# Kernel optimization log

Measured on AMD Instinct MI355X. Metric: run time of the kernel, lower is better.

## Reference

```python
import jax, jax.numpy as jnp
import numpy as np

NEG_SLOPE = 0.2
LN_EPS = 1e-5


def setup_inputs() -> dict:
    key = jax.random.key(0)
    ks = jax.random.split(key, 8)
    N, F, d, L, H = 100000, 128, 64, 3, 4
    dh = d // H
    E = 1600000
    return {
        "x": jax.random.normal(ks[0], (N, F), dtype=jnp.float32),
        "edge_index": jax.random.randint(ks[1], (2, E), 0, N, dtype=jnp.int64),
        "W_enc": jax.random.normal(ks[2], (F, d), dtype=jnp.float32) / np.sqrt(F),
        "b_enc": jnp.zeros((d,), jnp.float32),
        "Wl": jax.random.normal(ks[3], (L, d, d), dtype=jnp.float32) / np.sqrt(d),
        "bl": jnp.zeros((L, d), jnp.float32),
        "Wr": jax.random.normal(ks[4], (L, d, d), dtype=jnp.float32) / np.sqrt(d),
        "br": jnp.zeros((L, d), jnp.float32),
        "att": jax.random.normal(ks[5], (L, H, dh), dtype=jnp.float32) / np.sqrt(dh),
        "out_bias": jnp.zeros((L, d), jnp.float32),
        "gamma": jnp.ones((L, d), jnp.float32),
        "beta": jnp.zeros((L, d), jnp.float32),
    }


def _elu(x):
    return jnp.where(x > 0, x, jnp.expm1(x))


def reference(x, edge_index, W_enc, b_enc, Wl, bl, Wr, br, att, out_bias, gamma, beta):
    N = x.shape[0]
    L, H, dh = att.shape
    d = H * dh
    # PyG GATv2Conv default add_self_loops=True
    loops = jnp.arange(N, dtype=edge_index.dtype)
    src = jnp.concatenate([edge_index[0], loops])  # message source
    dst = jnp.concatenate([edge_index[1], loops])  # aggregation target

    h = jax.nn.relu(x @ W_enc + b_enc)  # [N, d]
    for l in range(L):
        xl = (h @ Wl[l] + bl[l]).reshape(N, H, dh)
        xr = (h @ Wr[l] + br[l]).reshape(N, H, dh)
        # GATv2: score = a^T LeakyReLU(xl[src] + xr[dst])  -> [E, H]
        e = jax.nn.leaky_relu(xl[src] + xr[dst], NEG_SLOPE)
        score = jnp.einsum('ehd,hd->eh', e, att[l])
        # segment softmax over incoming edges of each dst node
        smax = jax.ops.segment_max(score, dst, num_segments=N)
        ex = jnp.exp(score - smax[dst])
        denom = jax.ops.segment_sum(ex, dst, num_segments=N)
        alpha = ex / denom[dst]  # [E, H]
        agg = jax.ops.segment_sum(alpha[:, :, None] * xl[src], dst, num_segments=N)
        hc = agg.reshape(N, d) + out_bias[l]
        # LayerNorm
        mu = hc.mean(-1, keepdims=True)
        var = ((hc - mu) ** 2).mean(-1, keepdims=True)
        hn = (hc - mu) * jax.lax.rsqrt(var + LN_EPS) * gamma[l] + beta[l]
        h = _elu(hn)  # dropout p=0.0 -> identity
    return h
```

## Files before the change

kernel.cpp:

```cpp
#include <hip/hip_runtime.h>
#include <hip/hip_fp16.h>
#include <math.h>

static constexpr int D = 64;
static constexpr int F = 128;
static constexpr int BK = 64;
static constexpr float NEG_SLOPE = 0.2f;
static constexpr float LN_EPS = 1e-5f;
static constexpr float LOG2E = 1.44269504088896340736f;
static constexpr int NCHUNK = 8;

template <int CTRL>
__device__ __forceinline__ float dpp_add(float x) {
  int v = __builtin_amdgcn_update_dpp(0, __float_as_int(x), CTRL, 0xF, 0xF, true);
  return x + __int_as_float(v);
}
__device__ __forceinline__ float red8(float x) {
  x = dpp_add<0xB1>(x);
  x = dpp_add<0x4E>(x);
  x = dpp_add<0x141>(x);
  return x;
}
__device__ __forceinline__ float red16(float x) {
  x = red8(x);
  x = dpp_add<0x140>(x);
  return x;
}
__device__ __forceinline__ float red32(float x) {
  x = red16(x);
  x += __shfl_xor(x, 16);
  return x;
}

__device__ __forceinline__ __half2 h2max(__half2 a, __half2 b) {
  int ai = __builtin_bit_cast(int, a), bi = __builtin_bit_cast(int, b), r;
  asm("v_pk_max_f16 %0, %1, %2" : "=v"(r) : "v"(ai), "v"(bi));
  return __builtin_bit_cast(__half2, r);
}

typedef _Float16 half2_t __attribute__((ext_vector_type(2)));
__device__ __forceinline__ float fdot2f(__half2 a, __half2 b) {
#if __has_builtin(__builtin_amdgcn_fdot2)
  return __builtin_amdgcn_fdot2(__builtin_bit_cast(half2_t, a),
                                __builtin_bit_cast(half2_t, b), 0.f, false);
#else
  float2 af = __half22float2(a), bf = __half22float2(b);
  return fmaf(af.x, bf.x, af.y * bf.y);
#endif
}


__global__ __launch_bounds__(256) void k_init_buckets(int* __restrict__ cursor,
                                                      int* __restrict__ ssrc, int N) {
  int tid = blockIdx.x * 256 + threadIdx.x;
  int total = N * (BK / 4) + 4;
  if (tid < total) {
    int row = tid >> 4;
    int sub = tid & 15;
    int4 v = make_int4(0, 0, 0, 0);
    if (sub == 0 && row < N) v.x = row;
    ((int4*)ssrc)[tid] = v;
  }
  if (tid < N) cursor[tid] = 1;
}

__global__ __launch_bounds__(256) void k_scatter(const int* __restrict__ src,
                                                 const int* __restrict__ dst,
                                                 int* __restrict__ cursor,
                                                 int* __restrict__ ssrc, int E, int N) {
  int c = blockIdx.x & (NCHUNK - 1);
  int b0 = (c * N) / NCHUNK, b1 = ((c + 1) * N) / NCHUNK;
  int stride = (gridDim.x / NCHUNK) * 256;
  for (int e = (blockIdx.x >> 3) * 256 + threadIdx.x; e < E; e += stride) {
    int d = dst[e];
    if (d >= b0 && d < b1) {
      int p = atomicAdd(&cursor[d], 1);
      if (p < BK) ssrc[(d << 6) + p] = src[e];
    }
  }
}


__global__ __launch_bounds__(256) void k_encoder(const float* __restrict__ x,
                                                 const float* __restrict__ W,
                                                 const float* __restrict__ b,
                                                 float* __restrict__ h, int N) {
  __shared__ float xT[F][64];
  __shared__ float Ws[F][64];
  int t = threadIdx.x;
  int n0 = blockIdx.x * 64;
  for (int i = t; i < F * D / 4; i += 256)
    ((float4*)&Ws[0][0])[i] = ((const float4*)W)[i];
  {
    int r = t & 63, kq = (t >> 6) * 4;
    int n = n0 + r;
#pragma unroll
    for (int i = 0; i < 8; ++i) {
      int k0 = kq + 16 * i;
      float4 v = (n < N) ? *(const float4*)&x[(size_t)n * F + k0]
                         : make_float4(0.f, 0.f, 0.f, 0.f);
      xT[k0][r] = v.x; xT[k0 + 1][r] = v.y; xT[k0 + 2][r] = v.z; xT[k0 + 3][r] = v.w;
    }
  }
  __syncthreads();
  int c4 = (t & 15) * 4, n4 = (t >> 4) * 4;
  float acc[4][4];
#pragma unroll
  for (int i = 0; i < 4; ++i)
#pragma unroll
    for (int j = 0; j < 4; ++j) acc[i][j] = b[c4 + j];
#pragma unroll 4
  for (int k = 0; k < F; ++k) {
    float4 xv = *(const float4*)&xT[k][n4];
    float4 wv = *(const float4*)&Ws[k][c4];
    const float* xp = (const float*)&xv;
    const float* wp = (const float*)&wv;
#pragma unroll
    for (int i = 0; i < 4; ++i)
#pragma unroll
      for (int j = 0; j < 4; ++j) acc[i][j] = fmaf(xp[i], wp[j], acc[i][j]);
  }
#pragma unroll
  for (int i = 0; i < 4; ++i) {
    int n = n0 + n4 + i;
    if (n < N) {
      float4 o = make_float4(fmaxf(acc[i][0], 0.f), fmaxf(acc[i][1], 0.f),
                             fmaxf(acc[i][2], 0.f), fmaxf(acc[i][3], 0.f));
      *(float4*)&h[(size_t)n * D + c4] = o;
    }
  }
}


__global__ __launch_bounds__(256) void k_layer_gemm(const float* __restrict__ h,
                                                    const float* __restrict__ Wl,
                                                    const float* __restrict__ bl,
                                                    const float* __restrict__ Wr,
                                                    const float* __restrict__ br,
                                                    ushort* __restrict__ xlh,
                                                    float* __restrict__ xr, int N) {
  __shared__ float hT[D][64];
  __shared__ float Wls[D][64];
  __shared__ float Wrs[D][64];
  int t = threadIdx.x;
  int n0 = blockIdx.x * 64;
  for (int i = t; i < D * D / 4; i += 256) {
    ((float4*)&Wls[0][0])[i] = ((const float4*)Wl)[i];
    ((float4*)&Wrs[0][0])[i] = ((const float4*)Wr)[i];
  }
  {
    int r = t & 63, kq = (t >> 6) * 4;
    int n = n0 + r;
#pragma unroll
    for (int i = 0; i < 4; ++i) {
      int k0 = kq + 16 * i;
      float4 v = (n < N) ? *(const float4*)&h[(size_t)n * D + k0]
                         : make_float4(0.f, 0.f, 0.f, 0.f);
      hT[k0][r] = v.x; hT[k0 + 1][r] = v.y; hT[k0 + 2][r] = v.z; hT[k0 + 3][r] = v.w;
    }
  }
  __syncthreads();
  int c4 = (t & 15) * 4, n4 = (t >> 4) * 4;
  float aL[4][4], aR[4][4];
#pragma unroll
  for (int i = 0; i < 4; ++i)
#pragma unroll
    for (int j = 0; j < 4; ++j) { aL[i][j] = bl[c4 + j]; aR[i][j] = br[c4 + j]; }
#pragma unroll 4
  for (int k = 0; k < D; ++k) {
    float4 xv = *(const float4*)&hT[k][n4];
    float4 lv = *(const float4*)&Wls[k][c4];
    float4 rv = *(const float4*)&Wrs[k][c4];
    const float* xp = (const float*)&xv;
    const float* lp = (const float*)&lv;
    const float* rp = (const float*)&rv;
#pragma unroll
    for (int i = 0; i < 4; ++i)
#pragma unroll
      for (int j = 0; j < 4; ++j) {
        aL[i][j] = fmaf(xp[i], lp[j], aL[i][j]);
        aR[i][j] = fmaf(xp[i], rp[j], aR[i][j]);
      }
  }
#pragma unroll
  for (int i = 0; i < 4; ++i) {
    int n = n0 + n4 + i;
    if (n < N) {
      ushort4 o;
      o.x = __half_as_ushort(__float2half_rn(aL[i][0]));
      o.y = __half_as_ushort(__float2half_rn(aL[i][1]));
      o.z = __half_as_ushort(__float2half_rn(aL[i][2]));
      o.w = __half_as_ushort(__float2half_rn(aL[i][3]));
      *(ushort4*)&xlh[(size_t)n * D + c4] = o;
      *(float4*)&xr[(size_t)n * D + c4] =
          make_float4(aR[i][0], aR[i][1], aR[i][2], aR[i][3]);
    }
  }
}


template <int P>
__device__ __forceinline__ void batchH(const char* __restrict__ xlb,
                                       const int* __restrict__ srow,
                                       int slot0, int cnt, int voff, int nd,
                                       __half2 xr2, __half2 a2, __half2 ns2,
                                       float& m, float& s, float& a0, float& a1) {
  int sj[P];
#pragma unroll
  for (int g = 0; g < P / 4; ++g) {
    int4 q = *(const int4*)(srow + slot0 + 4 * g);
    sj[4 * g + 0] = q.x; sj[4 * g + 1] = q.y;
    sj[4 * g + 2] = q.z; sj[4 * g + 3] = q.w;
  }
#pragma unroll
  for (int j = 0; j < P; ++j)
    if (slot0 + j >= cnt) sj[j] = nd;
  __half2 xsv[P];
  float p[P];
#pragma unroll
  for (int j = 0; j < P; ++j)
    xsv[j] = *(const __half2*)(xlb + (((uint32_t)sj[j] << 7) | (uint32_t)voff));
#pragma unroll
  for (int j = 0; j < P; ++j) {
    __half2 v2 = __hadd2(xsv[j], xr2);
    __half2 lr2 = h2max(v2, __hmul2(v2, ns2));
    float pj = red8(fdot2f(a2, lr2));
    p[j] = (slot0 + j < cnt) ? pj : -3.0e38f;
  }
  float pmax = p[0];
#pragma unroll
  for (int j = 1; j < P; ++j) pmax = fmaxf(pmax, p[j]);
  float mnew = fmaxf(m, pmax);
  float c = __builtin_amdgcn_exp2f(m - mnew);
  s *= c; a0 *= c; a1 *= c;
#pragma unroll
  for (int j = 0; j < P; ++j) {
    float w = __builtin_amdgcn_exp2f(p[j] - mnew);
    s += w;
    a0 = fmaf(w, __low2float(xsv[j]), a0);
    a1 = fmaf(w, __high2float(xsv[j]), a1);
  }
  m = mnew;
}

__global__ __launch_bounds__(256) void k_edge_layer(const __half* __restrict__ xlh,
                                                    const float* __restrict__ xr,
                                                    const int* __restrict__ cnt_arr,
                                                    const int* __restrict__ ssrc,
                                                    const float* __restrict__ att_l,
                                                    const float* __restrict__ ob_l,
                                                    const float* __restrict__ g_l,
                                                    const float* __restrict__ be_l,
                                                    float* __restrict__ out, int N) {
  int lane = threadIdx.x & 63;
  int c2 = lane & 31, half = lane >> 5;
  int voff = c2 * 4;
  int wid = threadIdx.x >> 6;
  int wave = blockIdx.x * 4 + wid;
  int nw = gridDim.x * 4;
  const char* xlb = (const char*)xlh;
  float2 af = make_float2(att_l[2 * c2] * LOG2E, att_l[2 * c2 + 1] * LOG2E);
  __half2 a2 = __float22half2_rn(af);
  __half2 ns2 = __float2half2_rn(NEG_SLOPE);
  float2 ob = *(const float2*)&ob_l[2 * c2];
  float2 gm = *(const float2*)&g_l[2 * c2];
  float2 bt = *(const float2*)&be_l[2 * c2];
  int npairs = (N + 1) >> 1;
  for (int ip = wave; ip < npairs; ip += nw) {
    int node = 2 * ip + half;
    bool valid = node < N;
    int nd = valid ? node : N - 1;
    __half2 xr2 = __float22half2_rn(*(const float2*)&xr[(size_t)nd * D + 2 * c2]);
    int cnt = min(cnt_arr[nd], BK);
    const int* srow = ssrc + (nd << 6);
    float m = -1.0e30f, s = 0.f, a0 = 0.f, a1 = 0.f;
    batchH<16>(xlb, srow, 0, cnt, voff, nd, xr2, a2, ns2, m, s, a0, a1);
    for (int slot = 16; slot < cnt; slot += 4)
      batchH<4>(xlb, srow, slot, cnt, voff, nd, xr2, a2, ns2, m, s, a0, a1);
    float rs = __builtin_amdgcn_rcpf(s);
    float r0 = fmaf(a0, rs, ob.x);
    float r1 = fmaf(a1, rs, ob.y);
    float mu = red32(r0 + r1) * (1.f / 64.f);
    float d0 = r0 - mu, d1 = r1 - mu;
    float var = red32(fmaf(d0, d0, d1 * d1)) * (1.f / 64.f);
    float rstd = rsqrtf(var + LN_EPS);
    float h0 = fmaf(d0 * rstd, gm.x, bt.x);
    float h1 = fmaf(d1 * rstd, gm.y, bt.y);
    h0 = h0 > 0.f ? h0 : expm1f(h0);
    h1 = h1 > 0.f ? h1 : expm1f(h1);
    if (valid)
      *(float2*)&out[(size_t)node * D + 2 * c2] = make_float2(h0, h1);
  }
}


extern "C" void kernel_launch(void* const* d_in, const int* in_sizes, int n_in,
                              void* d_out, int out_size, void* d_ws, size_t ws_size,
                              hipStream_t stream) {
  const float* x      = (const float*)d_in[0];
  const int*   ei     = (const int*)d_in[1];
  const float* W_enc  = (const float*)d_in[2];
  const float* b_enc  = (const float*)d_in[3];
  const float* Wl     = (const float*)d_in[4];
  const float* bl     = (const float*)d_in[5];
  const float* Wr     = (const float*)d_in[6];
  const float* br     = (const float*)d_in[7];
  const float* att    = (const float*)d_in[8];
  const float* obias  = (const float*)d_in[9];
  const float* gamma  = (const float*)d_in[10];
  const float* beta   = (const float*)d_in[11];

  int N = in_sizes[0] / F;
  int E = in_sizes[1] / 2;
  const int* src = ei;
  const int* dst = ei + E;

  auto align = [](size_t v) { return (v + 255) & ~(size_t)255; };
  char* ws = (char*)d_ws;
  float* h  = (float*)ws;   ws += align((size_t)N * D * 4);
  ushort* xlh = (ushort*)ws; ws += align((size_t)N * D * 2);
  float* xr = (float*)ws;   ws += align((size_t)N * D * 4);
  int* cursor = (int*)ws;   ws += align((size_t)N * 4);
  int* ssrc   = (int*)ws;   ws += align(((size_t)N * BK + 16) * 4);

  int tblk = (N + 63) / 64;
  int iblk = (N * (BK / 4) + 4 + 255) / 256;

  k_init_buckets<<<iblk, 256, 0, stream>>>(cursor, ssrc, N);
  k_scatter<<<2048, 256, 0, stream>>>(src, dst, cursor, ssrc, E, N);

  k_encoder<<<tblk, 256, 0, stream>>>(x, W_enc, b_enc, h, N);

  for (int l = 0; l < 3; ++l) {
    k_layer_gemm<<<tblk, 256, 0, stream>>>(h, Wl + l * D * D, bl + l * D,
                                           Wr + l * D * D, br + l * D, xlh, xr, N);
    float* out = (l == 2) ? (float*)d_out : h;
    k_edge_layer<<<2048, 256, 0, stream>>>((const __half*)xlh, xr, cursor, ssrc,
                                           att + l * 64, obias + l * 64,
                                           gamma + l * 64, beta + l * 64, out, N);
  }
}
```

Before: 363.3 us.

## Partition edges into per-chunk queues before bucket scatter

Replaces the scatter kernel, which had every chunk's blocks rescan the full edge list and filter by destination range, with a two-pass scheme. A partition kernel reads each edge once, assigns it to a destination chunk using a magic-number multiply, and appends (dst, src) pairs to per-chunk queues via shared-memory counters plus one global atomic per chunk. A second kernel then scatters each chunk's queue into the adjacency buckets. This cuts the redundant reads of the edge list but adds an extra kernel launch and a queue buffer write and read. Queue capacity is fixed at E/NCHUNK plus slack, so a skewed destination distribution would silently drop edges.

```diff
diff --git a/kernel.cpp b/kernel.cpp
--- a/kernel.cpp
+++ b/kernel.cpp
@@ -51,7 +51,8 @@
 
 
 __global__ __launch_bounds__(256) void k_init_buckets(int* __restrict__ cursor,
-                                                      int* __restrict__ ssrc, int N) {
+                                                      int* __restrict__ ssrc,
+                                                      int* __restrict__ qcnt, int N) {
   int tid = blockIdx.x * 256 + threadIdx.x;
   int total = N * (BK / 4) + 4;
   if (tid < total) {
@@ -62,21 +63,69 @@
     ((int4*)ssrc)[tid] = v;
   }
   if (tid < N) cursor[tid] = 1;
-}
-
-__global__ __launch_bounds__(256) void k_scatter(const int* __restrict__ src,
-                                                 const int* __restrict__ dst,
-                                                 int* __restrict__ cursor,
-                                                 int* __restrict__ ssrc, int E, int N) {
+  if (tid < NCHUNK) qcnt[tid] = 0;
+}
+
+__global__ __launch_bounds__(256) void k_partition(const int* __restrict__ src,
+                                                   const int* __restrict__ dst,
+                                                   int* __restrict__ qcnt,
+                                                   int2* __restrict__ queue,
+                                                   int qcap, int E, uint32_t magic) {
+  __shared__ int qc[NCHUNK];
+  __shared__ int qb[NCHUNK];
+  int t = threadIdx.x;
+  if (t < NCHUNK) qc[t] = 0;
+  __syncthreads();
+  int base = blockIdx.x * 1024 + t * 4;
+  int sv[4], dv[4], c[4], pl[4];
+  bool ok[4];
+  if (base + 3 < E) {
+    int4 s4 = *(const int4*)(src + base);
+    int4 d4 = *(const int4*)(dst + base);
+    sv[0] = s4.x; sv[1] = s4.y; sv[2] = s4.z; sv[3] = s4.w;
+    dv[0] = d4.x; dv[1] = d4.y; dv[2] = d4.z; dv[3] = d4.w;
+#pragma unroll
+    for (int k = 0; k < 4; ++k) ok[k] = true;
+  } else {
+#pragma unroll
+    for (int k = 0; k < 4; ++k) {
+      ok[k] = base + k < E;
+      sv[k] = ok[k] ? src[base + k] : 0;
+      dv[k] = ok[k] ? dst[base + k] : 0;
+    }
+  }
+#pragma unroll
+  for (int k = 0; k < 4; ++k) {
+    if (ok[k]) {
+      c[k] = __umulhi((uint32_t)dv[k], magic);
+      pl[k] = atomicAdd(&qc[c[k]], 1);
+    }
+  }
+  __syncthreads();
+  if (t < NCHUNK) qb[t] = (qc[t] > 0) ? atomicAdd(&qcnt[t], qc[t]) : 0;
+  __syncthreads();
+#pragma unroll
+  for (int k = 0; k < 4; ++k) {
+    if (ok[k]) {
+      int pos = qb[c[k]] + pl[k];
+      if (pos < qcap) queue[(size_t)c[k] * qcap + pos] = make_int2(dv[k], sv[k]);
+    }
+  }
+}
+
+__global__ __launch_bounds__(256) void k_scatter2(const int* __restrict__ qcnt,
+                                                  const int2* __restrict__ queue,
+                                                  int qcap,
+                                                  int* __restrict__ cursor,
+                                                  int* __restrict__ ssrc) {
   int c = blockIdx.x & (NCHUNK - 1);
-  int b0 = (c * N) / NCHUNK, b1 = ((c + 1) * N) / NCHUNK;
+  int nq = qcnt[c];
+  const int2* q = queue + (size_t)c * qcap;
   int stride = (gridDim.x / NCHUNK) * 256;
-  for (int e = (blockIdx.x >> 3) * 256 + threadIdx.x; e < E; e += stride) {
-    int d = dst[e];
-    if (d >= b0 && d < b1) {
-      int p = atomicAdd(&cursor[d], 1);
-      if (p < BK) ssrc[(d << 6) + p] = src[e];
-    }
+  for (int i = (blockIdx.x >> 3) * 256 + threadIdx.x; i < nq; i += stride) {
+    int2 e = q[i];
+    int p = atomicAdd(&cursor[e.x], 1);
+    if (p < BK) ssrc[(e.x << 6) + p] = e.y;
   }
 }
 
@@ -322,12 +371,18 @@
   float* xr = (float*)ws;   ws += align((size_t)N * D * 4);
   int* cursor = (int*)ws;   ws += align((size_t)N * 4);
   int* ssrc   = (int*)ws;   ws += align(((size_t)N * BK + 16) * 4);
+  int* qcnt   = (int*)ws;   ws += align((size_t)NCHUNK * 4);
+  int qcap = E / NCHUNK + 16384;
+  int2* queue = (int2*)ws;  ws += align((size_t)NCHUNK * qcap * 8);
 
   int tblk = (N + 63) / 64;
   int iblk = (N * (BK / 4) + 4 + 255) / 256;
-
-  k_init_buckets<<<iblk, 256, 0, stream>>>(cursor, ssrc, N);
-  k_scatter<<<2048, 256, 0, stream>>>(src, dst, cursor, ssrc, E, N);
+  int pblk = (E + 1023) / 1024;
+  uint32_t magic = (uint32_t)((((uint64_t)NCHUNK) << 32) / (uint64_t)N + 1);
+
+  k_init_buckets<<<iblk, 256, 0, stream>>>(cursor, ssrc, qcnt, N);
+  k_partition<<<pblk, 256, 0, stream>>>(src, dst, qcnt, queue, qcap, E, magic);
+  k_scatter2<<<2048, 256, 0, stream>>>(qcnt, queue, qcap, cursor, ssrc);
 
   k_encoder<<<tblk, 256, 0, stream>>>(x, W_enc, b_enc, h, N);
 
```

Result: slower. 386.5 us (median of 2 runs) (+6.4%).
